# Kernel tuning notes

Measured on AMD Instinct MI355X. Metric: run time of the kernel, lower is better.

The kernel has to match this reference:

```python
import jax, jax.numpy as jnp
import numpy as np
from jax import lax

PAD = 2          # shift_size // 2
CHUNKS = 5       # shift_size


def shift(x, H, W, D, axis):
    # x: (B, N, C) with N = H*W*D; axis in {2,3,4} of the (B,C,H,W,D) view
    B, N, C = x.shape
    xn = x.transpose(0, 2, 1).reshape(B, C, H, W, D)
    xn = jnp.pad(xn, ((0, 0), (0, 0), (PAD, PAD), (PAD, PAD), (PAD, PAD)))
    xs = jnp.split(xn, CHUNKS, axis=1)
    rolled = [jnp.roll(xc, s, axis) for xc, s in zip(xs, range(-PAD, PAD + 1))]
    xc = jnp.concatenate(rolled, axis=1)
    xc = xc[:, :, PAD:PAD + H, PAD:PAD + W, PAD:PAD + D]
    return xc.reshape(B, C, H * W * D).transpose(0, 2, 1)


def dwconv(x, k, b, H, W, D):
    # depthwise 3x3x3 conv; x: (B,N,C), k: (C,1,3,3,3), b: (C,)
    B, N, C = x.shape
    v = x.transpose(0, 2, 1).reshape(B, C, H, W, D)
    y = lax.conv_general_dilated(
        v, k, window_strides=(1, 1, 1), padding='SAME',
        feature_group_count=C,
        dimension_numbers=('NCDHW', 'OIDHW', 'NCDHW'))
    y = y + b[None, :, None, None, None]
    return y.reshape(B, C, N).transpose(0, 2, 1)


def setup_inputs() -> dict:
    key = jax.random.key(0)
    ks = jax.random.split(key, 12)
    B, H, W, D = 4, 32, 32, 32
    C = 160  # in = hidden = out
    N = H * W * D
    inp = {
        'x': jax.random.normal(ks[0], (B, N, C), jnp.float32),
        'H': H, 'W': W, 'D': D,
        'w1': jax.random.normal(ks[1], (C, C), jnp.float32) * 0.02,
        'b1': jnp.zeros((C,), jnp.float32),
        'dw1': jax.random.normal(ks[2], (C, 1, 3, 3, 3), jnp.float32) * 0.27,
        'bdw1': jnp.zeros((C,), jnp.float32),
        'w2': jax.random.normal(ks[3], (C, C), jnp.float32) * 0.02,
        'b2': jnp.zeros((C,), jnp.float32),
        'dw2': jax.random.normal(ks[4], (C, 1, 3, 3, 3), jnp.float32) * 0.27,
        'bdw2': jnp.zeros((C,), jnp.float32),
        'w3': jax.random.normal(ks[5], (C, C), jnp.float32) * 0.02,
        'b3': jnp.zeros((C,), jnp.float32),
    }
    return inp


def reference(x, H, W, D, w1, b1, dw1, bdw1, w2, b2, dw2, bdw2, w3, b3):
    x = shift(x, H, W, D, axis=2)
    x = x @ w1 + b1                       # fc1 (drop p=0)
    x = dwconv(x, dw1, bdw1, H, W, D)
    x = shift(x, H, W, D, axis=3)
    x = x @ w2 + b2                       # fc2
    x = dwconv(x, dw2, bdw2, H, W, D)
    x = shift(x, H, W, D, axis=4)
    x = x @ w3 + b3                       # fc3
    x = jax.nn.gelu(x, approximate=False) # nn.GELU default (exact erf)
    return x
```

## Files before the change

### kernel.cpp

```cpp
#include <hip/hip_runtime.h>

typedef __bf16 bf16x8 __attribute__((ext_vector_type(8)));
typedef float f32x4 __attribute__((ext_vector_type(4)));

__device__ inline unsigned short f2bf(float f) {
    unsigned x = __builtin_bit_cast(unsigned, f);
    x += 0x7fffu + ((x >> 16) & 1u);
    return (unsigned short)(x >> 16);
}
__device__ inline unsigned pack2bf(float lo, float hi) {
    return (unsigned)f2bf(lo) | ((unsigned)f2bf(hi) << 16);
}
__device__ inline void cvt8(uint4 u, float* o) {
    o[0] = __builtin_bit_cast(float, u.x << 16);
    o[1] = __builtin_bit_cast(float, u.x & 0xffff0000u);
    o[2] = __builtin_bit_cast(float, u.y << 16);
    o[3] = __builtin_bit_cast(float, u.y & 0xffff0000u);
    o[4] = __builtin_bit_cast(float, u.z << 16);
    o[5] = __builtin_bit_cast(float, u.z & 0xffff0000u);
    o[6] = __builtin_bit_cast(float, u.w << 16);
    o[7] = __builtin_bit_cast(float, u.w & 0xffff0000u);
}
__device__ inline float gelu_f(float v) {
    float x = fabsf(v) * 0.70710678118654752f;
    float td = __builtin_amdgcn_rcpf(1.0f + 0.3275911f * x);
    float p = ((((1.061405429f * td - 1.453152027f) * td + 1.421413741f) * td
                - 0.284496736f) * td + 0.254829592f) * td;
    float e = __expf(-x * x);
    float er = 1.0f - p * e;
    float s = v < 0.0f ? -er : er;
    return 0.5f * v * (1.0f + s);
}

__device__ inline void gload_lds16(const void* g, void* l) {
    typedef __attribute__((address_space(1))) const unsigned int gq;
    typedef __attribute__((address_space(3))) unsigned int sq;
    __builtin_amdgcn_global_load_lds((gq*)g, (sq*)l, 16, 0, 0);
}

#define WPAD 164
#define WELEMS (160 * WPAD)
#define WCHUNKS (WELEMS * 2 / 16)

__global__ __launch_bounds__(256) void prep_w3(const float* __restrict__ W1,
                                               const float* __restrict__ W2,
                                               const float* __restrict__ W3,
                                               unsigned short* __restrict__ dst) {
    int e = blockIdx.x * 256 + threadIdx.x;
    if (e >= 3 * WELEMS) return;
    int m = e / WELEMS;
    int r = e - m * WELEMS;
    int co = r / WPAD, ci = r - co * WPAD;
    const float* W = (m == 0) ? W1 : (m == 1) ? W2 : W3;
    dst[e] = (ci < 160) ? f2bf(W[ci * 160 + co]) : (unsigned short)0;
}

template <int AXIS, bool FP32IN>
__device__ inline void load_a_raw(const void* __restrict__ Xv, int row, uint4* u,
                                  float4* f, int kq) {
    const int n = row & 32767;
    const int coord = (AXIS == 0) ? (n >> 10) : (AXIS == 1) ? ((n >> 5) & 31) : (n & 31);
    const int stride = (AXIS == 0) ? 1024 : (AXIS == 1) ? 32 : 1;
#pragma unroll
    for (int g = 0; g < 5; g++) {
        int s = 2 - g;
        bool ok = (unsigned)(coord + s) < 32u;
        int srow = ok ? row + s * stride : row;
        size_t off = (size_t)srow * 160 + g * 32 + kq * 8;
        if (FP32IN) {
            const float* p = (const float*)Xv + off;
            float4 r0 = ((const float4*)p)[0];
            float4 r1 = ((const float4*)p)[1];
            if (!ok) { r0 = make_float4(0, 0, 0, 0); r1 = make_float4(0, 0, 0, 0); }
            f[g * 2] = r0; f[g * 2 + 1] = r1;
        } else {
            uint4 v = *(const uint4*)((const unsigned short*)Xv + off);
            if (!ok) v = make_uint4(0, 0, 0, 0);
            u[g] = v;
        }
    }
}

template <bool FP32IN>
__device__ inline void pack_a(const uint4* u, const float4* f, uint4* a) {
#pragma unroll
    for (int g = 0; g < 5; g++) {
        if (FP32IN) {
            float4 r0 = f[g * 2], r1 = f[g * 2 + 1];
            a[g] = make_uint4(pack2bf(r0.x, r0.y), pack2bf(r0.z, r0.w),
                              pack2bf(r1.x, r1.y), pack2bf(r1.z, r1.w));
        } else {
            a[g] = u[g];
        }
    }
}

__device__ inline void tile_compute_both(const unsigned short* __restrict__ lw,
                                         const uint4* a0, const uint4* a1,
                                         f32x4* acc0, f32x4* acc1, int mr, int kq) {
#pragma unroll
    for (int g = 0; g < 5; g++) {
        bf16x8 x0 = __builtin_bit_cast(bf16x8, a0[g]);
        bf16x8 x1 = __builtin_bit_cast(bf16x8, a1[g]);
        const unsigned short* bp = lw + mr * WPAD + g * 32 + kq * 8;
#pragma unroll
        for (int nt = 0; nt < 10; nt++) {
            bf16x8 wf = __builtin_bit_cast(bf16x8, *(const uint4*)(bp + nt * 16 * WPAD));
            acc0[nt] = __builtin_amdgcn_mfma_f32_16x16x32_bf16(wf, x0, acc0[nt], 0, 0, 0);
            acc1[nt] = __builtin_amdgcn_mfma_f32_16x16x32_bf16(wf, x1, acc1[nt], 0, 0, 0);
        }
    }
}

template <bool GELU, bool F32OUT>
__device__ inline void stage_store(unsigned short* __restrict__ lbase,
                                   const f32x4* acc, const float* __restrict__ Bs,
                                   void* __restrict__ Yv, int rowbase,
                                   int lane, int slot, int mr, int kq) {
    if (F32OUT) {
        float* sw = (float*)lbase + slot * (16 * 164);
#pragma unroll
        for (int nt = 0; nt < 10; nt++) {
            float4 bb = *(const float4*)(Bs + nt * 16 + kq * 4);
            float v0 = acc[nt][0] + bb.x, v1 = acc[nt][1] + bb.y,
                  v2 = acc[nt][2] + bb.z, v3 = acc[nt][3] + bb.w;
            if (GELU) { v0 = gelu_f(v0); v1 = gelu_f(v1); v2 = gelu_f(v2); v3 = gelu_f(v3); }
            *(float4*)(sw + mr * 164 + nt * 16 + kq * 4) = make_float4(v0, v1, v2, v3);
        }
#pragma unroll
        for (int p = 0; p < 10; p++) {
            int idx = p * 256 + lane * 4;
            int row = idx / 160;
            int col = idx - row * 160;
            float4 v = *(const float4*)(sw + row * 164 + col);
            *(float4*)((float*)Yv + (size_t)rowbase * 160 + idx) = v;
        }
    } else {
        unsigned short* sw = lbase + slot * (16 * 168);
#pragma unroll
        for (int nt = 0; nt < 10; nt++) {
            float4 bb = *(const float4*)(Bs + nt * 16 + kq * 4);
            float v0 = acc[nt][0] + bb.x, v1 = acc[nt][1] + bb.y,
                  v2 = acc[nt][2] + bb.z, v3 = acc[nt][3] + bb.w;
            if (GELU) { v0 = gelu_f(v0); v1 = gelu_f(v1); v2 = gelu_f(v2); v3 = gelu_f(v3); }
            uint2 pk;
            pk.x = pack2bf(v0, v1);
            pk.y = pack2bf(v2, v3);
            *(uint2*)(sw + mr * 168 + nt * 16 + kq * 4) = pk;
        }
#pragma unroll
        for (int p = 0; p < 5; p++) {
            int idx = p * 512 + lane * 8;
            int row = idx / 160;
            int col = idx - row * 160;
            uint4 v = *(const uint4*)(sw + row * 168 + col);
            *(uint4*)((unsigned short*)Yv + (size_t)rowbase * 160 + idx) = v;
        }
    }
}

template <int AXIS, bool GELU, bool FP32IN, bool F32OUT>
__global__ __launch_bounds__(256, 3) void gemm_shift(
    const void* __restrict__ Xv, const unsigned short* __restrict__ Wt,
    const float* __restrict__ Bs, void* __restrict__ Yv) {
    __shared__ unsigned short lw[WELEMS];
    const int t = threadIdx.x;
    const int lane = t & 63, wv = t >> 6, mr = lane & 15, kq = lane >> 4;
    const int rbase = blockIdx.x * 128;

    for (int i = t; i < WCHUNKS; i += 256)
        gload_lds16((const char*)Wt + i * 16, (char*)lw + i * 16);

    uint4 u0[5], u1[5];
    float4 f0[10], f1[10];
    load_a_raw<AXIS, FP32IN>(Xv, rbase + wv * 16 + mr, u0, f0, kq);
    load_a_raw<AXIS, FP32IN>(Xv, rbase + 64 + wv * 16 + mr, u1, f1, kq);

    __syncthreads();

    uint4 a0[5], a1[5];
    pack_a<FP32IN>(u0, f0, a0);
    pack_a<FP32IN>(u1, f1, a1);
    f32x4 acc0[10] = {};
    f32x4 acc1[10] = {};
    tile_compute_both(lw, a0, a1, acc0, acc1, mr, kq);

    __syncthreads();
    const int slot0 = wv;
    const int slot1 = F32OUT ? wv : wv + 4;
    stage_store<GELU, F32OUT>(lw, acc0, Bs, Yv, rbase + wv * 16, lane, slot0, mr, kq);
    stage_store<GELU, F32OUT>(lw, acc1, Bs, Yv, rbase + 64 + wv * 16, lane, slot1, mr, kq);
}

__global__ __launch_bounds__(256) void dwconv3(
    const unsigned short* __restrict__ X, const float* __restrict__ Kw,
    const float* __restrict__ Bs, unsigned short* __restrict__ Y) {
    __shared__ float wl[20 * 220];
    const int t = threadIdx.x;
    for (int e = t; e < 160 * 27; e += 256) {
        int c = e / 27, tap = e % 27;
        wl[(c >> 3) * 220 + tap * 8 + (c & 7)] = Kw[e];
    }
    __syncthreads();

    int bid = blockIdx.x;
    int swz = (bid & 7) * 320 + (bid >> 3);
    int idx = swz * 256 + t;

    int cc = idx % 20;
    int r = idx / 20;
    int dq = r & 7;  r >>= 3;
    int w = r & 31;  r >>= 5;
    int h = r & 31;
    int b = r >> 5;
    int d0 = dq << 2;

    float acc[4][8];
    {
        float bv[8];
        *(float4*)&bv[0] = ((const float4*)(Bs + cc * 8))[0];
        *(float4*)&bv[4] = ((const float4*)(Bs + cc * 8))[1];
#pragma unroll
        for (int od = 0; od < 4; od++)
#pragma unroll
            for (int j = 0; j < 8; j++) acc[od][j] = bv[j];
    }
    const float* wbase = &wl[cc * 220];
#pragma unroll
    for (int dh = -1; dh <= 1; dh++) {
        int hh = h + dh;
        if ((unsigned)hh >= 32u) continue;
#pragma unroll
        for (int dwi = -1; dwi <= 1; dwi++) {
            int ww = w + dwi;
            if ((unsigned)ww >= 32u) continue;
            const unsigned short* base =
                X + (size_t)(b * 32768 + hh * 1024 + ww * 32) * 160 + cc * 8;
            int tap0 = (dh + 1) * 9 + (dwi + 1) * 3;
            float wv_[24];
#pragma unroll
            for (int q2 = 0; q2 < 6; q2++)
                ((float4*)wv_)[q2] = *(const float4*)(wbase + tap0 * 8 + q2 * 4);
            uint4 ub[6];
#pragma unroll
            for (int dd = 0; dd < 6; dd++) {
                int d = d0 - 1 + dd;
                ub[dd] = ((unsigned)d < 32u) ? *(const uint4*)(base + d * 160)
                                             : make_uint4(0, 0, 0, 0);
            }
            float vb[6][8];
#pragma unroll
            for (int dd = 0; dd < 6; dd++) cvt8(ub[dd], vb[dd]);
#pragma unroll
            for (int od = 0; od < 4; od++)
#pragma unroll
                for (int dd = 0; dd < 3; dd++)
#pragma unroll
                    for (int j = 0; j < 8; j++)
                        acc[od][j] += vb[od + dd][j] * wv_[dd * 8 + j];
        }
    }
#pragma unroll
    for (int od = 0; od < 4; od++) {
        unsigned short tmp[8];
#pragma unroll
        for (int j = 0; j < 8; j++) tmp[j] = f2bf(acc[od][j]);
        *(uint4*)(Y + (size_t)(b * 32768 + h * 1024 + w * 32 + d0 + od) * 160 + cc * 8) =
            *(uint4*)tmp;
    }
}

extern "C" void kernel_launch(void* const* d_in, const int* in_sizes, int n_in,
                              void* d_out, int out_size, void* d_ws, size_t ws_size,
                              hipStream_t stream) {
    const void*  x    = d_in[0];
    const float* w1   = (const float*)d_in[4];
    const float* b1   = (const float*)d_in[5];
    const float* dw1  = (const float*)d_in[6];
    const float* bdw1 = (const float*)d_in[7];
    const float* w2   = (const float*)d_in[8];
    const float* b2   = (const float*)d_in[9];
    const float* dw2  = (const float*)d_in[10];
    const float* bdw2 = (const float*)d_in[11];
    const float* w3   = (const float*)d_in[12];
    const float* b3   = (const float*)d_in[13];

    unsigned short* wbf = (unsigned short*)d_ws;

    const size_t BUF_BYTES = (size_t)4 * 32768 * 160 * 2;
    const size_t OFF_A = 2u << 20;
    const size_t OFF_B = OFF_A + BUF_BYTES;
    unsigned short* bufA;
    unsigned short* bufB;
    if (ws_size >= OFF_B + BUF_BYTES) {
        bufA = (unsigned short*)((char*)d_ws + OFF_A);
        bufB = (unsigned short*)((char*)d_ws + OFF_B);
    } else {
        bufA = (unsigned short*)d_out;
        bufB = (unsigned short*)d_in[0];
    }

    prep_w3<<<(3 * WELEMS + 255) / 256, 256, 0, stream>>>(w1, w2, w3, wbf);
    gemm_shift<0, false, true,  false><<<1024, 256, 0, stream>>>(x,    wbf,              b1, bufA);
    dwconv3<<<2560, 256, 0, stream>>>(bufA, dw1, bdw1, bufB);
    gemm_shift<1, false, false, false><<<1024, 256, 0, stream>>>(bufB, wbf + WELEMS,     b2, bufA);
    dwconv3<<<2560, 256, 0, stream>>>(bufA, dw2, bdw2, bufB);
    gemm_shift<2, true,  false, true ><<<1024, 256, 0, stream>>>(bufB, wbf + 2 * WELEMS, b3, d_out);
}
```

Measured before the change: 350.2 us.

## Process two row tiles per GEMM block with prefetch and direct f32 stores

Each GEMM block now handles 256 rows instead of 128, so the LDS weight load is amortized over twice the work, and the second tile's activations are loaded before the first tile's MFMAs run. Output staging moves to a dedicated LDS buffer so the barrier before storing is removed, and the fp32 GELU output is written straight from registers without staging. The weight row pad changes to 168 and the occupancy hint drops to 2 blocks per CU. The cost is higher register and LDS use per block, half as many blocks, and less coalesced fp32 stores.

```diff
diff --git a/kernel.cpp b/kernel.cpp
--- a/kernel.cpp
+++ b/kernel.cpp
@@ -38,7 +38,7 @@
     __builtin_amdgcn_global_load_lds((gq*)g, (sq*)l, 16, 0, 0);
 }
 
-#define WPAD 164
+#define WPAD 168
 #define WELEMS (160 * WPAD)
 #define WCHUNKS (WELEMS * 2 / 16)
 
@@ -112,61 +112,54 @@
     }
 }
 
-template <bool GELU, bool F32OUT>
-__device__ inline void stage_store(unsigned short* __restrict__ lbase,
-                                   const f32x4* acc, const float* __restrict__ Bs,
-                                   void* __restrict__ Yv, int rowbase,
-                                   int lane, int slot, int mr, int kq) {
-    if (F32OUT) {
-        float* sw = (float*)lbase + slot * (16 * 164);
-#pragma unroll
-        for (int nt = 0; nt < 10; nt++) {
-            float4 bb = *(const float4*)(Bs + nt * 16 + kq * 4);
-            float v0 = acc[nt][0] + bb.x, v1 = acc[nt][1] + bb.y,
-                  v2 = acc[nt][2] + bb.z, v3 = acc[nt][3] + bb.w;
-            if (GELU) { v0 = gelu_f(v0); v1 = gelu_f(v1); v2 = gelu_f(v2); v3 = gelu_f(v3); }
-            *(float4*)(sw + mr * 164 + nt * 16 + kq * 4) = make_float4(v0, v1, v2, v3);
-        }
-#pragma unroll
-        for (int p = 0; p < 10; p++) {
-            int idx = p * 256 + lane * 4;
-            int row = idx / 160;
-            int col = idx - row * 160;
-            float4 v = *(const float4*)(sw + row * 164 + col);
-            *(float4*)((float*)Yv + (size_t)rowbase * 160 + idx) = v;
-        }
-    } else {
-        unsigned short* sw = lbase + slot * (16 * 168);
-#pragma unroll
-        for (int nt = 0; nt < 10; nt++) {
-            float4 bb = *(const float4*)(Bs + nt * 16 + kq * 4);
-            float v0 = acc[nt][0] + bb.x, v1 = acc[nt][1] + bb.y,
-                  v2 = acc[nt][2] + bb.z, v3 = acc[nt][3] + bb.w;
-            if (GELU) { v0 = gelu_f(v0); v1 = gelu_f(v1); v2 = gelu_f(v2); v3 = gelu_f(v3); }
-            uint2 pk;
-            pk.x = pack2bf(v0, v1);
-            pk.y = pack2bf(v2, v3);
-            *(uint2*)(sw + mr * 168 + nt * 16 + kq * 4) = pk;
-        }
-#pragma unroll
-        for (int p = 0; p < 5; p++) {
-            int idx = p * 512 + lane * 8;
-            int row = idx / 160;
-            int col = idx - row * 160;
-            uint4 v = *(const uint4*)(sw + row * 168 + col);
-            *(uint4*)((unsigned short*)Yv + (size_t)rowbase * 160 + idx) = v;
-        }
+__device__ inline void store_bf16_staged(unsigned short* __restrict__ stg,
+                                         const f32x4* acc, const float* __restrict__ Bs,
+                                         unsigned short* __restrict__ Yv, int rowbase,
+                                         int lane, int wv, int mr, int kq) {
+    unsigned short* sw = stg + wv * (16 * 168);
+#pragma unroll
+    for (int nt = 0; nt < 10; nt++) {
+        float4 bb = *(const float4*)(Bs + nt * 16 + kq * 4);
+        uint2 pk;
+        pk.x = pack2bf(acc[nt][0] + bb.x, acc[nt][1] + bb.y);
+        pk.y = pack2bf(acc[nt][2] + bb.z, acc[nt][3] + bb.w);
+        *(uint2*)(sw + mr * 168 + nt * 16 + kq * 4) = pk;
+    }
+#pragma unroll
+    for (int p = 0; p < 5; p++) {
+        int idx = p * 512 + lane * 8;
+        int row = idx / 160;
+        int col = idx - row * 160;
+        uint4 v = *(const uint4*)(sw + row * 168 + col);
+        *(uint4*)(Yv + (size_t)rowbase * 160 + idx) = v;
+    }
+}
+
+__device__ inline void store_f32_direct(const f32x4* acc, const float* __restrict__ Bs,
+                                        float* __restrict__ Yv, int rowbase,
+                                        int mr, int kq) {
+    float* rp = Yv + (size_t)(rowbase + mr) * 160;
+#pragma unroll
+    for (int nt = 0; nt < 10; nt++) {
+        float4 bb = *(const float4*)(Bs + nt * 16 + kq * 4);
+        float4 v;
+        v.x = gelu_f(acc[nt][0] + bb.x);
+        v.y = gelu_f(acc[nt][1] + bb.y);
+        v.z = gelu_f(acc[nt][2] + bb.z);
+        v.w = gelu_f(acc[nt][3] + bb.w);
+        *(float4*)(rp + nt * 16 + kq * 4) = v;
     }
 }
 
 template <int AXIS, bool GELU, bool FP32IN, bool F32OUT>
-__global__ __launch_bounds__(256, 3) void gemm_shift(
+__global__ __launch_bounds__(256, 2) void gemm_shift(
     const void* __restrict__ Xv, const unsigned short* __restrict__ Wt,
     const float* __restrict__ Bs, void* __restrict__ Yv) {
     __shared__ unsigned short lw[WELEMS];
+    __shared__ unsigned short stg[F32OUT ? 1 : 4 * 16 * 168];
     const int t = threadIdx.x;
     const int lane = t & 63, wv = t >> 6, mr = lane & 15, kq = lane >> 4;
-    const int rbase = blockIdx.x * 128;
+    const int rbase = blockIdx.x * 256;
 
     for (int i = t; i < WCHUNKS; i += 256)
         gload_lds16((const char*)Wt + i * 16, (char*)lw + i * 16);
@@ -181,15 +174,33 @@
     uint4 a0[5], a1[5];
     pack_a<FP32IN>(u0, f0, a0);
     pack_a<FP32IN>(u1, f1, a1);
+
+    load_a_raw<AXIS, FP32IN>(Xv, rbase + 128 + wv * 16 + mr, u0, f0, kq);
+    load_a_raw<AXIS, FP32IN>(Xv, rbase + 192 + wv * 16 + mr, u1, f1, kq);
+
     f32x4 acc0[10] = {};
     f32x4 acc1[10] = {};
     tile_compute_both(lw, a0, a1, acc0, acc1, mr, kq);
-
-    __syncthreads();
-    const int slot0 = wv;
-    const int slot1 = F32OUT ? wv : wv + 4;
-    stage_store<GELU, F32OUT>(lw, acc0, Bs, Yv, rbase + wv * 16, lane, slot0, mr, kq);
-    stage_store<GELU, F32OUT>(lw, acc1, Bs, Yv, rbase + 64 + wv * 16, lane, slot1, mr, kq);
+    if (F32OUT) {
+        store_f32_direct(acc0, Bs, (float*)Yv, rbase + wv * 16, mr, kq);
+        store_f32_direct(acc1, Bs, (float*)Yv, rbase + 64 + wv * 16, mr, kq);
+    } else {
+        store_bf16_staged(stg, acc0, Bs, (unsigned short*)Yv, rbase + wv * 16, lane, wv, mr, kq);
+        store_bf16_staged(stg, acc1, Bs, (unsigned short*)Yv, rbase + 64 + wv * 16, lane, wv, mr, kq);
+    }
+
+    pack_a<FP32IN>(u0, f0, a0);
+    pack_a<FP32IN>(u1, f1, a1);
+#pragma unroll
+    for (int nt = 0; nt < 10; nt++) { acc0[nt] = f32x4{0, 0, 0, 0}; acc1[nt] = f32x4{0, 0, 0, 0}; }
+    tile_compute_both(lw, a0, a1, acc0, acc1, mr, kq);
+    if (F32OUT) {
+        store_f32_direct(acc0, Bs, (float*)Yv, rbase + 128 + wv * 16, mr, kq);
+        store_f32_direct(acc1, Bs, (float*)Yv, rbase + 192 + wv * 16, mr, kq);
+    } else {
+        store_bf16_staged(stg, acc0, Bs, (unsigned short*)Yv, rbase + 128 + wv * 16, lane, wv, mr, kq);
+        store_bf16_staged(stg, acc1, Bs, (unsigned short*)Yv, rbase + 192 + wv * 16, lane, wv, mr, kq);
+    }
 }
 
 __global__ __launch_bounds__(256) void dwconv3(
@@ -300,10 +311,10 @@
         bufB = (unsigned short*)d_in[0];
     }
 
-    prep_w3<<<(3 * WELEMS + 255) / 256, 256, 0, stream>>>(w1, w2, w3, wbf);
-    gemm_shift<0, false, true,  false><<<1024, 256, 0, stream>>>(x,    wbf,              b1, bufA);
+    prep_w3<<<315, 256, 0, stream>>>(w1, w2, w3, wbf);
+    gemm_shift<0, false, true,  false><<<512, 256, 0, stream>>>(x,    wbf,              b1, bufA);
     dwconv3<<<2560, 256, 0, stream>>>(bufA, dw1, bdw1, bufB);
-    gemm_shift<1, false, false, false><<<1024, 256, 0, stream>>>(bufB, wbf + WELEMS,     b2, bufA);
+    gemm_shift<1, false, false, false><<<512, 256, 0, stream>>>(bufB, wbf + WELEMS,     b2, bufA);
     dwconv3<<<2560, 256, 0, stream>>>(bufA, dw2, bdw2, bufB);
-    gemm_shift<2, true,  false, true ><<<1024, 256, 0, stream>>>(bufB, wbf + 2 * WELEMS, b3, d_out);
-}
+    gemm_shift<2, true,  false, true ><<<512, 256, 0, stream>>>(bufB, wbf + 2 * WELEMS, b3, d_out);
+}
```

Measured after the change: 303.5 us. -13.3%, faster.
